# Kernel tuning notes

Hardware: AMD Instinct MI355X
Metric: run time of the kernel (lower is better)

The kernel has to match this reference:

```python
import jax, jax.numpy as jnp
import numpy as np

B, S, D_SEQ, D_ITEM, A, H = 2048, 200, 256, 64, 128, 1
HD = A // H
SCALE = A ** 0.5


def prelu(x, a):
    return jnp.where(x >= 0, x, a * x)


def setup_inputs() -> dict:
    key = jax.random.key(0)
    ks = jax.random.split(key, 10)
    inp = {
        "transformer_out": jax.random.normal(ks[0], (B, S, D_SEQ), dtype=jnp.float32),
        "mask": jax.random.randint(ks[1], (B, S), 0, 2, dtype=jnp.int32),  # 1 = pad
        "target_item_emb": jax.random.normal(ks[2], (B, D_ITEM), dtype=jnp.float32),
        # parameters (torch Linear weight layout: [out, in])
        "W_q": jax.random.normal(ks[3], (A, D_ITEM), dtype=jnp.float32) * (1.0 / np.sqrt(D_ITEM)),
        "W_k": jax.random.normal(ks[4], (A, D_SEQ), dtype=jnp.float32) * (1.0 / np.sqrt(D_SEQ)),
        "W_v": jax.random.normal(ks[5], (A, D_SEQ), dtype=jnp.float32) * (1.0 / np.sqrt(D_SEQ)),
        "W_kernel": jnp.eye(HD, dtype=jnp.float32),
        "ffn_W": jax.random.normal(ks[6], (D_SEQ, A), dtype=jnp.float32) * (1.0 / np.sqrt(A)),
        "ffn_b": jnp.zeros((D_SEQ,), dtype=jnp.float32),
        "prelu_a": jnp.asarray(0.25, dtype=jnp.float32),  # shared PReLU(1) param
    }
    return inp


def reference(transformer_out, mask, target_item_emb, W_q, W_k, W_v, W_kernel, ffn_W, ffn_b, prelu_a):
    # Q/K/V projections + shared PReLU activation
    K = prelu(jnp.einsum('bsd,ad->bsa', transformer_out, W_k), prelu_a)   # [B,S,A]
    V = prelu(jnp.einsum('bsd,ad->bsa', transformer_out, W_v), prelu_a)   # [B,S,A]
    Q = prelu(jnp.einsum('bd,ad->ba', target_item_emb, W_q), prelu_a)     # [B,A]

    # split heads
    Kh = K.reshape(B, S, H, HD)          # [B,S,H,hd]
    Vh = V.reshape(B, S, H, HD)
    Qh = Q.reshape(B, H, HD)             # [B,H,hd]

    # bilinear attention score: K W Q^T / sqrt(attn_dim)
    score = jnp.einsum('bshd,dc,bhc->bhs', Kh, W_kernel, Qh) / SCALE      # [B,H,S]

    # mask: input mask 1=pad; valid = 1-mask; padded positions -> -1e9
    valid = (1 - mask).astype(jnp.float32)[:, None, :]                     # [B,1,S]
    score = jnp.where(valid == 0, -1e9, score)

    attn = jax.nn.softmax(score, axis=-1)                                  # [B,H,S]

    # weighted sum of values, merge heads
    out = jnp.einsum('bhs,bshd->bhd', attn, Vh).reshape(B, H * HD)         # [B,A]

    ffn_out = prelu(out @ ffn_W.T + ffn_b, prelu_a)                        # [B,D_SEQ]
    return ffn_out, attn
```

## Files before the change

kernel.cpp:

```cpp
#include <hip/hip_runtime.h>
#include <hip/hip_bf16.h>

#define NB    2048
#define SS    200
#define DSEQ  256
#define DITEM 64
#define AA    128
#define NS    4

typedef __bf16 bf16x8 __attribute__((ext_vector_type(8)));
typedef float  f32x4  __attribute__((ext_vector_type(4)));

__device__ __forceinline__ float prelu_f(float x, float a) { return x >= 0.f ? x : a * x; }

#define ROR_F(x, n) __int_as_float(__builtin_amdgcn_update_dpp(0, __float_as_int(x), 0x120 + (n), 0xf, 0xf, true))
__device__ __forceinline__ float row_sum16(float x) {
    x += ROR_F(x, 1); x += ROR_F(x, 2); x += ROR_F(x, 4); x += ROR_F(x, 8);
    return x;
}
__device__ __forceinline__ float row_max16(float x) {
    x = fmaxf(x, ROR_F(x, 1)); x = fmaxf(x, ROR_F(x, 2));
    x = fmaxf(x, ROR_F(x, 4)); x = fmaxf(x, ROR_F(x, 8));
    return x;
}

__global__ void prep_kernel(const float* __restrict__ Wk, const float* __restrict__ Wv,
                            __hip_bfloat16* __restrict__ Wb) {
    int idx = blockIdx.x * 256 + threadIdx.x;
    int a = idx >> 8, d = idx & 255;
    float v = (a < 128) ? Wk[a * 256 + d] : Wv[(a - 128) * 256 + d];
    int boff = (d * 2) ^ ((a & 7) << 4);
    Wb[a * 256 + (boff >> 1)] = __float2bfloat16(v);
}

#define ISSUE_R(tt, s, L, H)                                                    \
    {                                                                           \
        int r_ = idx_lds[s][(tt) * 16 + srow];                                  \
        const float* xp_ = X + ((size_t)(b0 + (s)) * SS + r_) * DSEQ + chunk * 8; \
        L = *reinterpret_cast<const f32x4*>(xp_);                               \
        H = *reinterpret_cast<const f32x4*>(xp_ + 4);                           \
    }

#define STAGE_R(tt, s, L, H)                                                    \
    {                                                                           \
        bf16x8 v_;                                                              \
        v_[0] = (__bf16)L[0]; v_[1] = (__bf16)L[1];                             \
        v_[2] = (__bf16)L[2]; v_[3] = (__bf16)L[3];                             \
        v_[4] = (__bf16)H[0]; v_[5] = (__bf16)H[1];                             \
        v_[6] = (__bf16)H[2]; v_[7] = (__bf16)H[3];                             \
        *reinterpret_cast<bf16x8*>(xbase + (s) * 16384 + ((tt) & 1) * 8192 + wr_off) = v_; \
    }

#define SMFOLD(tp, s)                                                           \
    {                                                                           \
        const int q_ = (tp) & 1;                                                \
        const int s0_ = (tp) * 16;                                              \
        f32x4 r0_ = *reinterpret_cast<const f32x4*>(&sp[s][q_][c][0]);          \
        f32x4 r1_ = *reinterpret_cast<const f32x4*>(&sp[s][q_][c][4]);          \
        float sc_ = (r0_[0]+r0_[1]+r0_[2]+r0_[3]+r1_[0]+r1_[1]+r1_[2]+r1_[3]) * inv_scale; \
        sc_ = (s0_ + c < nv##s) ? sc_ : -1e9f;                                  \
        if (tid < 16 && s0_ + tid < nv##s) arena[s][idx_lds[s][s0_ + tid]] = sc_; \
        float tmax_ = row_max16(sc_);                                           \
        float nm_ = fmaxf(m##s, tmax_);                                         \
        float fs_ = __expf(m##s - nm_);                                         \
        float e_  = __expf(sc_ - nm_);                                          \
        float ls_ = row_sum16(e_);                                              \
        l##s = l##s * fs_ + ls_; m##s = nm_;                                    \
        oacc##s *= fs_;                                                         \
        _Pragma("unroll")                                                       \
        for (int i_ = 0; i_ < 4; i_++) {                                        \
            float ew_ = __shfl(e_, (lane & 48) | (rg * 4 + i_), 64);            \
            oacc##s += ew_ * prelu_f(aVp##s[i_], pa);                           \
        }                                                                       \
    }

#define CHALF(k0)                                                               \
    _Pragma("unroll")                                                           \
    for (int k = (k0); k < (k0) + 4; k++) {                                     \
        const int o = (k * 64 + rg * 16) ^ rswz;                                \
        bf16x8 bk  = *reinterpret_cast<const bf16x8*>(kb + o);                  \
        bf16x8 bv  = *reinterpret_cast<const bf16x8*>(vb + o);                  \
        bf16x8 af0 = *reinterpret_cast<const bf16x8*>(rb0 + o);                 \
        bf16x8 af1 = *reinterpret_cast<const bf16x8*>(rb1 + o);                 \
        bf16x8 af2 = *reinterpret_cast<const bf16x8*>(rb2 + o);                 \
        bf16x8 af3 = *reinterpret_cast<const bf16x8*>(rb3 + o);                 \
        aK0 = __builtin_amdgcn_mfma_f32_16x16x32_bf16(af0, bk, aK0, 0, 0, 0);   \
        aVp0 = __builtin_amdgcn_mfma_f32_16x16x32_bf16(af0, bv, aVp0, 0, 0, 0); \
        aK1 = __builtin_amdgcn_mfma_f32_16x16x32_bf16(af1, bk, aK1, 0, 0, 0);   \
        aVp1 = __builtin_amdgcn_mfma_f32_16x16x32_bf16(af1, bv, aVp1, 0, 0, 0); \
        aK2 = __builtin_amdgcn_mfma_f32_16x16x32_bf16(af2, bk, aK2, 0, 0, 0);   \
        aVp2 = __builtin_amdgcn_mfma_f32_16x16x32_bf16(af2, bv, aVp2, 0, 0, 0); \
        aK3 = __builtin_amdgcn_mfma_f32_16x16x32_bf16(af3, bk, aK3, 0, 0, 0);   \
        aVp3 = __builtin_amdgcn_mfma_f32_16x16x32_bf16(af3, bv, aVp3, 0, 0, 0); \
    }

#define SCOREPART(tt, s)                                                        \
    {                                                                           \
        float pr_[4];                                                           \
        _Pragma("unroll")                                                       \
        for (int i = 0; i < 4; i++) pr_[i] = row_sum16(prelu_f(aK##s[i], pa) * uw##s); \
        if (c == 0) {                                                           \
            _Pragma("unroll")                                                   \
            for (int i = 0; i < 4; i++) sp[s][(tt) & 1][rg * 4 + i][w] = pr_[i]; \
        }                                                                       \
    }

__global__ __launch_bounds__(512, 2)
void pool_main(
    const float* __restrict__ X,
    const int*   __restrict__ maskp,
    const float* __restrict__ temb,
    const float* __restrict__ Wq,
    const float* __restrict__ Wker,
    const float* __restrict__ ffnW,
    const float* __restrict__ ffnb,
    const float* __restrict__ prelu_a,
    const __hip_bfloat16* __restrict__ Wb,
    float* __restrict__ out)
{
    __shared__ __hip_bfloat16 Xt[NS][2][16][256];
    __shared__ float sp[NS][2][16][8];
    __shared__ float arena[NS][336];
    __shared__ int   idx_lds[NS][208];
    __shared__ int   nvt[NS];

    const int tid  = threadIdx.x;
    const int w    = tid >> 6;
    const int lane = tid & 63;
    const int c    = lane & 15;
    const int rg   = lane >> 4;
    const int b0   = blockIdx.x * NS;
    const float pa = *prelu_a;
    const float inv_scale = 0.08838834764831845f;

    const int srow  = tid >> 5;
    const int chunk = tid & 31;
    const int wr_off = srow * 512 + ((chunk * 16) ^ ((srow & 7) << 4));
    char* xbase = (char*)&Xt[0][0][0][0];
    const int rswz = (c & 7) << 4;

    const char* kb = (const char*)Wb + (size_t)(16 * w + c) * 512;
    const char* vb = kb + 65536;

    if (w < NS) {
        int base = 0;
        #pragma unroll
        for (int ch = 0; ch < 4; ch++) {
            int pos = ch * 64 + lane;
            bool val = (pos < SS) && (maskp[(size_t)(b0 + w) * SS + pos] == 0);
            unsigned long long ball = __ballot(val);
            int pre = __popcll(ball & ((1ull << lane) - 1));
            if (val) idx_lds[w][base + pre] = pos;
            base += (int)__popcll(ball);
        }
        asm volatile("s_waitcnt lgkmcnt(0)" ::: "memory");
        int safe = (base > 0) ? idx_lds[w][base - 1] : 0;
        for (int j = base + lane; j < 208; j += 64) idx_lds[w][j] = safe;
        if (lane == 0) nvt[w] = base;
    }
    const int ps = tid >> 7;
    const int po = tid & 127;
    if (po < DITEM) arena[ps][po] = temb[(size_t)(b0 + ps) * DITEM + po];
    __syncthreads();

    f32x4 p0lo, p0hi, p1lo, p1hi, p2lo, p2hi, p3lo, p3hi;
    ISSUE_R(0, 0, p0lo, p0hi); ISSUE_R(0, 1, p1lo, p1hi);
    ISSUE_R(0, 2, p2lo, p2hi); ISSUE_R(0, 3, p3lo, p3hi);

    {
        float acc = 0.f;
        #pragma unroll
        for (int d4 = 0; d4 < 16; d4++) {
            f32x4 tv = *reinterpret_cast<const f32x4*>(&arena[ps][d4 * 4]);
            f32x4 wq4 = *reinterpret_cast<const f32x4*>(Wq + (size_t)po * DITEM + d4 * 4);
            acc += wq4[0]*tv[0] + wq4[1]*tv[1] + wq4[2]*tv[2] + wq4[3]*tv[3];
        }
        arena[ps][64 + po] = prelu_f(acc, pa);
    }
    __syncthreads();

    {
        float acc = 0.f;
        #pragma unroll
        for (int d4 = 0; d4 < 32; d4++) {
            f32x4 qv = *reinterpret_cast<const f32x4*>(&arena[ps][64 + d4 * 4]);
            f32x4 wk4 = *reinterpret_cast<const f32x4*>(Wker + (size_t)po * AA + d4 * 4);
            acc += wk4[0]*qv[0] + wk4[1]*qv[1] + wk4[2]*qv[2] + wk4[3]*qv[3];
        }
        arena[ps][192 + po] = acc;
    }
    __syncthreads();
    const float uw0 = arena[0][192 + 16 * w + c];
    const float uw1 = arena[1][192 + 16 * w + c];
    const float uw2 = arena[2][192 + 16 * w + c];
    const float uw3 = arena[3][192 + 16 * w + c];
    const int nv0 = nvt[0], nv1 = nvt[1], nv2 = nvt[2], nv3 = nvt[3];
    int ntmax = (nv0 + 15) >> 4;
    { int n1 = (nv1 + 15) >> 4; if (n1 > ntmax) ntmax = n1; }
    { int n2 = (nv2 + 15) >> 4; if (n2 > ntmax) ntmax = n2; }
    { int n3 = (nv3 + 15) >> 4; if (n3 > ntmax) ntmax = n3; }
    if (ntmax < 1) ntmax = 1;

    if (tid < 208) {
        arena[0][tid] = -1e9f; arena[1][tid] = -1e9f;
        arena[2][tid] = -1e9f; arena[3][tid] = -1e9f;
    }

    STAGE_R(0, 0, p0lo, p0hi); STAGE_R(0, 1, p1lo, p1hi);
    STAGE_R(0, 2, p2lo, p2hi); STAGE_R(0, 3, p3lo, p3hi);
    __syncthreads();

    float m0 = -INFINITY, l0 = 0.f, oacc0 = 0.f;
    float m1 = -INFINITY, l1 = 0.f, oacc1 = 0.f;
    float m2 = -INFINITY, l2 = 0.f, oacc2 = 0.f;
    float m3 = -INFINITY, l3 = 0.f, oacc3 = 0.f;
    f32x4 aVp0 = {0.f,0.f,0.f,0.f}, aVp1 = {0.f,0.f,0.f,0.f};
    f32x4 aVp2 = {0.f,0.f,0.f,0.f}, aVp3 = {0.f,0.f,0.f,0.f};
    f32x4 stAlo, stAhi, stBlo, stBhi;

    for (int t = 0; t < ntmax; t++) {
        const int more = (t + 1 < ntmax);

        if (more) { ISSUE_R(t + 1, 0, stAlo, stAhi); ISSUE_R(t + 1, 1, stBlo, stBhi); }

        if (t > 0) { SMFOLD(t - 1, 0); SMFOLD(t - 1, 1); SMFOLD(t - 1, 2); SMFOLD(t - 1, 3); }
        aVp0 = (f32x4){0.f,0.f,0.f,0.f}; aVp1 = (f32x4){0.f,0.f,0.f,0.f};
        aVp2 = (f32x4){0.f,0.f,0.f,0.f}; aVp3 = (f32x4){0.f,0.f,0.f,0.f};

        const char* rb0 = xbase + 0 * 16384 + (t & 1) * 8192 + c * 512;
        const char* rb1 = xbase + 1 * 16384 + (t & 1) * 8192 + c * 512;
        const char* rb2 = xbase + 2 * 16384 + (t & 1) * 8192 + c * 512;
        const char* rb3 = xbase + 3 * 16384 + (t & 1) * 8192 + c * 512;
        f32x4 aK0 = {0.f,0.f,0.f,0.f}, aK1 = {0.f,0.f,0.f,0.f};
        f32x4 aK2 = {0.f,0.f,0.f,0.f}, aK3 = {0.f,0.f,0.f,0.f};

        CHALF(0);

        if (more) {
            STAGE_R(t + 1, 0, stAlo, stAhi); ISSUE_R(t + 1, 2, stAlo, stAhi);
            STAGE_R(t + 1, 1, stBlo, stBhi); ISSUE_R(t + 1, 3, stBlo, stBhi);
        }

        CHALF(4);

        SCOREPART(t, 0); SCOREPART(t, 1); SCOREPART(t, 2); SCOREPART(t, 3);

        if (more) { STAGE_R(t + 1, 2, stAlo, stAhi); STAGE_R(t + 1, 3, stBlo, stBhi); }
        __syncthreads();
    }

    {
        const int tl = ntmax - 1;
        SMFOLD(tl, 0); SMFOLD(tl, 1); SMFOLD(tl, 2); SMFOLD(tl, 3);
    }

    oacc0 += __shfl_xor(oacc0, 16, 64); oacc0 += __shfl_xor(oacc0, 32, 64);
    oacc1 += __shfl_xor(oacc1, 16, 64); oacc1 += __shfl_xor(oacc1, 32, 64);
    oacc2 += __shfl_xor(oacc2, 16, 64); oacc2 += __shfl_xor(oacc2, 32, 64);
    oacc3 += __shfl_xor(oacc3, 16, 64); oacc3 += __shfl_xor(oacc3, 32, 64);
    const float invl0 = 1.0f / l0, invl1 = 1.0f / l1;
    const float invl2 = 1.0f / l2, invl3 = 1.0f / l3;
    if (lane < 16) {
        arena[0][208 + 16 * w + lane] = oacc0 * invl0;
        arena[1][208 + 16 * w + lane] = oacc1 * invl1;
        arena[2][208 + 16 * w + lane] = oacc2 * invl2;
        arena[3][208 + 16 * w + lane] = oacc3 * invl3;
    }
    __syncthreads();

    if (tid < SS) {
        out[(size_t)NB * DSEQ + (size_t)(b0 + 0) * SS + tid] = __expf(arena[0][tid] - m0) * invl0;
        out[(size_t)NB * DSEQ + (size_t)(b0 + 1) * SS + tid] = __expf(arena[1][tid] - m1) * invl1;
        out[(size_t)NB * DSEQ + (size_t)(b0 + 2) * SS + tid] = __expf(arena[2][tid] - m2) * invl2;
        out[(size_t)NB * DSEQ + (size_t)(b0 + 3) * SS + tid] = __expf(arena[3][tid] - m3) * invl3;
    }

    {
        const int o  = tid & 255;
        const int sA = tid >> 8;
        float accA = ffnb[o], accB = accA;
        #pragma unroll 8
        for (int a4 = 0; a4 < 32; a4++) {
            f32x4 wv4 = *reinterpret_cast<const f32x4*>(ffnW + (size_t)o * AA + a4 * 4);
            f32x4 ovA = *reinterpret_cast<const f32x4*>(&arena[sA][208 + a4 * 4]);
            f32x4 ovB = *reinterpret_cast<const f32x4*>(&arena[sA + 2][208 + a4 * 4]);
            accA += wv4[0]*ovA[0] + wv4[1]*ovA[1] + wv4[2]*ovA[2] + wv4[3]*ovA[3];
            accB += wv4[0]*ovB[0] + wv4[1]*ovB[1] + wv4[2]*ovB[2] + wv4[3]*ovB[3];
        }
        out[(size_t)(b0 + sA) * DSEQ + o]     = prelu_f(accA, pa);
        out[(size_t)(b0 + sA + 2) * DSEQ + o] = prelu_f(accB, pa);
    }
}

extern "C" void kernel_launch(void* const* d_in, const int* in_sizes, int n_in,
                              void* d_out, int out_size, void* d_ws, size_t ws_size,
                              hipStream_t stream) {
    const float* X    = (const float*)d_in[0];
    const int*   mask = (const int*)  d_in[1];
    const float* temb = (const float*)d_in[2];
    const float* Wq   = (const float*)d_in[3];
    const float* Wk   = (const float*)d_in[4];
    const float* Wv   = (const float*)d_in[5];
    const float* Wker = (const float*)d_in[6];
    const float* ffnW = (const float*)d_in[7];
    const float* ffnb = (const float*)d_in[8];
    const float* pa   = (const float*)d_in[9];
    float* out = (float*)d_out;

    __hip_bfloat16* Wb = (__hip_bfloat16*)d_ws;

    prep_kernel<<<256, 256, 0, stream>>>(Wk, Wv, Wb);
    pool_main<<<NB / NS, 512, 0, stream>>>(X, mask, temb, Wq, Wker, ffnW, ffnb, pa, Wb, out);
}
```

Before: 116.6 us.

## Split fused pooling kernel into projection pass and separate softmax/FFN kernel

Removes the online softmax and value accumulation from the projection kernel. The first kernel now writes raw scores and PReLU'd V tiles as bf16 to a workspace. A second per-batch kernel does the masked softmax, the weighted V sum and the FFN. This shortens the main kernel's critical loop and register pressure, at the cost of an extra launch and about 100MB of V written to and reread from global memory.

```diff
diff --git a/kernel.cpp b/kernel.cpp
--- a/kernel.cpp
+++ b/kernel.cpp
@@ -7,8 +7,10 @@
 #define DITEM 64
 #define AA    128
 #define NS    4
+#define MAXNT 13
 
 typedef __bf16 bf16x8 __attribute__((ext_vector_type(8)));
+typedef __bf16 bf16x4 __attribute__((ext_vector_type(4)));
 typedef float  f32x4  __attribute__((ext_vector_type(4)));
 
 __device__ __forceinline__ float prelu_f(float x, float a) { return x >= 0.f ? x : a * x; }
@@ -16,11 +18,6 @@
 #define ROR_F(x, n) __int_as_float(__builtin_amdgcn_update_dpp(0, __float_as_int(x), 0x120 + (n), 0xf, 0xf, true))
 __device__ __forceinline__ float row_sum16(float x) {
     x += ROR_F(x, 1); x += ROR_F(x, 2); x += ROR_F(x, 4); x += ROR_F(x, 8);
-    return x;
-}
-__device__ __forceinline__ float row_max16(float x) {
-    x = fmaxf(x, ROR_F(x, 1)); x = fmaxf(x, ROR_F(x, 2));
-    x = fmaxf(x, ROR_F(x, 4)); x = fmaxf(x, ROR_F(x, 8));
     return x;
 }
 
@@ -49,29 +46,6 @@
         v_[4] = (__bf16)H[0]; v_[5] = (__bf16)H[1];                             \
         v_[6] = (__bf16)H[2]; v_[7] = (__bf16)H[3];                             \
         *reinterpret_cast<bf16x8*>(xbase + (s) * 16384 + ((tt) & 1) * 8192 + wr_off) = v_; \
-    }
-
-#define SMFOLD(tp, s)                                                           \
-    {                                                                           \
-        const int q_ = (tp) & 1;                                                \
-        const int s0_ = (tp) * 16;                                              \
-        f32x4 r0_ = *reinterpret_cast<const f32x4*>(&sp[s][q_][c][0]);          \
-        f32x4 r1_ = *reinterpret_cast<const f32x4*>(&sp[s][q_][c][4]);          \
-        float sc_ = (r0_[0]+r0_[1]+r0_[2]+r0_[3]+r1_[0]+r1_[1]+r1_[2]+r1_[3]) * inv_scale; \
-        sc_ = (s0_ + c < nv##s) ? sc_ : -1e9f;                                  \
-        if (tid < 16 && s0_ + tid < nv##s) arena[s][idx_lds[s][s0_ + tid]] = sc_; \
-        float tmax_ = row_max16(sc_);                                           \
-        float nm_ = fmaxf(m##s, tmax_);                                         \
-        float fs_ = __expf(m##s - nm_);                                         \
-        float e_  = __expf(sc_ - nm_);                                          \
-        float ls_ = row_sum16(e_);                                              \
-        l##s = l##s * fs_ + ls_; m##s = nm_;                                    \
-        oacc##s *= fs_;                                                         \
-        _Pragma("unroll")                                                       \
-        for (int i_ = 0; i_ < 4; i_++) {                                        \
-            float ew_ = __shfl(e_, (lane & 48) | (rg * 4 + i_), 64);            \
-            oacc##s += ew_ * prelu_f(aVp##s[i_], pa);                           \
-        }                                                                       \
     }
 
 #define CHALF(k0)                                                               \
@@ -85,13 +59,13 @@
         bf16x8 af2 = *reinterpret_cast<const bf16x8*>(rb2 + o);                 \
         bf16x8 af3 = *reinterpret_cast<const bf16x8*>(rb3 + o);                 \
         aK0 = __builtin_amdgcn_mfma_f32_16x16x32_bf16(af0, bk, aK0, 0, 0, 0);   \
-        aVp0 = __builtin_amdgcn_mfma_f32_16x16x32_bf16(af0, bv, aVp0, 0, 0, 0); \
+        aV0 = __builtin_amdgcn_mfma_f32_16x16x32_bf16(af0, bv, aV0, 0, 0, 0);   \
         aK1 = __builtin_amdgcn_mfma_f32_16x16x32_bf16(af1, bk, aK1, 0, 0, 0);   \
-        aVp1 = __builtin_amdgcn_mfma_f32_16x16x32_bf16(af1, bv, aVp1, 0, 0, 0); \
+        aV1 = __builtin_amdgcn_mfma_f32_16x16x32_bf16(af1, bv, aV1, 0, 0, 0);   \
         aK2 = __builtin_amdgcn_mfma_f32_16x16x32_bf16(af2, bk, aK2, 0, 0, 0);   \
-        aVp2 = __builtin_amdgcn_mfma_f32_16x16x32_bf16(af2, bv, aVp2, 0, 0, 0); \
+        aV2 = __builtin_amdgcn_mfma_f32_16x16x32_bf16(af2, bv, aV2, 0, 0, 0);   \
         aK3 = __builtin_amdgcn_mfma_f32_16x16x32_bf16(af3, bk, aK3, 0, 0, 0);   \
-        aVp3 = __builtin_amdgcn_mfma_f32_16x16x32_bf16(af3, bv, aVp3, 0, 0, 0); \
+        aV3 = __builtin_amdgcn_mfma_f32_16x16x32_bf16(af3, bv, aV3, 0, 0, 0);   \
     }
 
 #define SCOREPART(tt, s)                                                        \
@@ -105,18 +79,37 @@
         }                                                                       \
     }
 
+#define VSTORE(tt, s)                                                           \
+    {                                                                           \
+        bf16x4 vv_;                                                             \
+        vv_[0] = (__bf16)prelu_f(aV##s[0], pa);                                 \
+        vv_[1] = (__bf16)prelu_f(aV##s[1], pa);                                 \
+        vv_[2] = (__bf16)prelu_f(aV##s[2], pa);                                 \
+        vv_[3] = (__bf16)prelu_f(aV##s[3], pa);                                 \
+        *reinterpret_cast<bf16x4*>(Vbuf + ((size_t)(b0 + (s)) * MAXNT + (tt)) * 4096 \
+                                   + w * 512 + lane * 8) = vv_;                 \
+    }
+
+#define SCSUM(tp)                                                               \
+    if (w < NS && lane < 16) {                                                  \
+        const int q_ = (tp) & 1;                                                \
+        f32x4 r0_ = *reinterpret_cast<const f32x4*>(&sp[w][q_][lane][0]);       \
+        f32x4 r1_ = *reinterpret_cast<const f32x4*>(&sp[w][q_][lane][4]);       \
+        scores_ws[(size_t)(b0 + w) * 208 + (tp) * 16 + lane] =                  \
+            r0_[0]+r0_[1]+r0_[2]+r0_[3]+r1_[0]+r1_[1]+r1_[2]+r1_[3];            \
+    }
+
 __global__ __launch_bounds__(512, 2)
-void pool_main(
+void proj_a(
     const float* __restrict__ X,
     const int*   __restrict__ maskp,
     const float* __restrict__ temb,
     const float* __restrict__ Wq,
     const float* __restrict__ Wker,
-    const float* __restrict__ ffnW,
-    const float* __restrict__ ffnb,
     const float* __restrict__ prelu_a,
     const __hip_bfloat16* __restrict__ Wb,
-    float* __restrict__ out)
+    float* __restrict__ scores_ws,
+    char*  __restrict__ Vbuf)
 {
     __shared__ __hip_bfloat16 Xt[NS][2][16][256];
     __shared__ float sp[NS][2][16][8];
@@ -131,7 +124,6 @@
     const int rg   = lane >> 4;
     const int b0   = blockIdx.x * NS;
     const float pa = *prelu_a;
-    const float inv_scale = 0.08838834764831845f;
 
     const int srow  = tid >> 5;
     const int chunk = tid & 31;
@@ -201,21 +193,10 @@
     { int n3 = (nv3 + 15) >> 4; if (n3 > ntmax) ntmax = n3; }
     if (ntmax < 1) ntmax = 1;
 
-    if (tid < 208) {
-        arena[0][tid] = -1e9f; arena[1][tid] = -1e9f;
-        arena[2][tid] = -1e9f; arena[3][tid] = -1e9f;
-    }
-
     STAGE_R(0, 0, p0lo, p0hi); STAGE_R(0, 1, p1lo, p1hi);
     STAGE_R(0, 2, p2lo, p2hi); STAGE_R(0, 3, p3lo, p3hi);
     __syncthreads();
 
-    float m0 = -INFINITY, l0 = 0.f, oacc0 = 0.f;
-    float m1 = -INFINITY, l1 = 0.f, oacc1 = 0.f;
-    float m2 = -INFINITY, l2 = 0.f, oacc2 = 0.f;
-    float m3 = -INFINITY, l3 = 0.f, oacc3 = 0.f;
-    f32x4 aVp0 = {0.f,0.f,0.f,0.f}, aVp1 = {0.f,0.f,0.f,0.f};
-    f32x4 aVp2 = {0.f,0.f,0.f,0.f}, aVp3 = {0.f,0.f,0.f,0.f};
     f32x4 stAlo, stAhi, stBlo, stBhi;
 
     for (int t = 0; t < ntmax; t++) {
@@ -223,9 +204,7 @@
 
         if (more) { ISSUE_R(t + 1, 0, stAlo, stAhi); ISSUE_R(t + 1, 1, stBlo, stBhi); }
 
-        if (t > 0) { SMFOLD(t - 1, 0); SMFOLD(t - 1, 1); SMFOLD(t - 1, 2); SMFOLD(t - 1, 3); }
-        aVp0 = (f32x4){0.f,0.f,0.f,0.f}; aVp1 = (f32x4){0.f,0.f,0.f,0.f};
-        aVp2 = (f32x4){0.f,0.f,0.f,0.f}; aVp3 = (f32x4){0.f,0.f,0.f,0.f};
+        if (t > 0) SCSUM(t - 1);
 
         const char* rb0 = xbase + 0 * 16384 + (t & 1) * 8192 + c * 512;
         const char* rb1 = xbase + 1 * 16384 + (t & 1) * 8192 + c * 512;
@@ -233,6 +212,8 @@
         const char* rb3 = xbase + 3 * 16384 + (t & 1) * 8192 + c * 512;
         f32x4 aK0 = {0.f,0.f,0.f,0.f}, aK1 = {0.f,0.f,0.f,0.f};
         f32x4 aK2 = {0.f,0.f,0.f,0.f}, aK3 = {0.f,0.f,0.f,0.f};
+        f32x4 aV0 = {0.f,0.f,0.f,0.f}, aV1 = {0.f,0.f,0.f,0.f};
+        f32x4 aV2 = {0.f,0.f,0.f,0.f}, aV3 = {0.f,0.f,0.f,0.f};
 
         CHALF(0);
 
@@ -244,52 +225,105 @@
         CHALF(4);
 
         SCOREPART(t, 0); SCOREPART(t, 1); SCOREPART(t, 2); SCOREPART(t, 3);
+        VSTORE(t, 0); VSTORE(t, 1); VSTORE(t, 2); VSTORE(t, 3);
 
         if (more) { STAGE_R(t + 1, 2, stAlo, stAhi); STAGE_R(t + 1, 3, stBlo, stBhi); }
         __syncthreads();
     }
 
-    {
-        const int tl = ntmax - 1;
-        SMFOLD(tl, 0); SMFOLD(tl, 1); SMFOLD(tl, 2); SMFOLD(tl, 3);
-    }
-
-    oacc0 += __shfl_xor(oacc0, 16, 64); oacc0 += __shfl_xor(oacc0, 32, 64);
-    oacc1 += __shfl_xor(oacc1, 16, 64); oacc1 += __shfl_xor(oacc1, 32, 64);
-    oacc2 += __shfl_xor(oacc2, 16, 64); oacc2 += __shfl_xor(oacc2, 32, 64);
-    oacc3 += __shfl_xor(oacc3, 16, 64); oacc3 += __shfl_xor(oacc3, 32, 64);
-    const float invl0 = 1.0f / l0, invl1 = 1.0f / l1;
-    const float invl2 = 1.0f / l2, invl3 = 1.0f / l3;
-    if (lane < 16) {
-        arena[0][208 + 16 * w + lane] = oacc0 * invl0;
-        arena[1][208 + 16 * w + lane] = oacc1 * invl1;
-        arena[2][208 + 16 * w + lane] = oacc2 * invl2;
-        arena[3][208 + 16 * w + lane] = oacc3 * invl3;
-    }
-    __syncthreads();
+    SCSUM(ntmax - 1);
+}
+
+__global__ __launch_bounds__(256)
+void attn_ffn_b(
+    const int*   __restrict__ maskp,
+    const float* __restrict__ scores_ws,
+    const char*  __restrict__ Vbuf,
+    const float* __restrict__ ffnW,
+    const float* __restrict__ ffnb,
+    const float* __restrict__ prelu_a,
+    float* __restrict__ out)
+{
+    __shared__ int   idx[208];
+    __shared__ int   inv[208];
+    __shared__ int   nv_s;
+    __shared__ float ebuf[208];
+    __shared__ float ovec[AA];
+    __shared__ float red[256];
+    __shared__ float wr1[4], wr2[4];
+
+    const int b = blockIdx.x, tid = threadIdx.x;
+    const int w = tid >> 6, lane = tid & 63;
+    const float pa = *prelu_a;
+    const float inv_scale = 0.08838834764831845f;
+
+    if (w == 0) {
+        int base = 0;
+        #pragma unroll
+        for (int ch = 0; ch < 4; ch++) {
+            int pos = ch * 64 + lane;
+            bool val = (pos < SS) && (maskp[(size_t)b * SS + pos] == 0);
+            unsigned long long ball = __ballot(val);
+            int pre = __popcll(ball & ((1ull << lane) - 1));
+            if (val) { idx[base + pre] = pos; inv[pos] = base + pre; }
+            base += (int)__popcll(ball);
+        }
+        if (lane == 0) nv_s = base;
+    }
+    __syncthreads();
+    const int nv = nv_s;
+
+    float sc = -3e38f;
+    if (tid < nv) sc = scores_ws[(size_t)b * 208 + tid] * inv_scale;
+    float v = sc;
+    #pragma unroll
+    for (int o = 1; o < 64; o <<= 1) v = fmaxf(v, __shfl_xor(v, o, 64));
+    if (lane == 0) wr1[w] = v;
+    __syncthreads();
+    const float m = fmaxf(fmaxf(wr1[0], wr1[1]), fmaxf(wr1[2], wr1[3]));
+    float e = (tid < nv) ? __expf(sc - m) : 0.f;
+    if (tid < 208) ebuf[tid] = e;
+    float sv = e;
+    #pragma unroll
+    for (int o = 1; o < 64; o <<= 1) sv += __shfl_xor(sv, o, 64);
+    if (lane == 0) wr2[w] = sv;
+    __syncthreads();
+    const float l = wr2[0] + wr2[1] + wr2[2] + wr2[3];
+    const float invl = 1.0f / l;
 
     if (tid < SS) {
-        out[(size_t)NB * DSEQ + (size_t)(b0 + 0) * SS + tid] = __expf(arena[0][tid] - m0) * invl0;
-        out[(size_t)NB * DSEQ + (size_t)(b0 + 1) * SS + tid] = __expf(arena[1][tid] - m1) * invl1;
-        out[(size_t)NB * DSEQ + (size_t)(b0 + 2) * SS + tid] = __expf(arena[2][tid] - m2) * invl2;
-        out[(size_t)NB * DSEQ + (size_t)(b0 + 3) * SS + tid] = __expf(arena[3][tid] - m3) * invl3;
-    }
-
-    {
-        const int o  = tid & 255;
-        const int sA = tid >> 8;
-        float accA = ffnb[o], accB = accA;
-        #pragma unroll 8
-        for (int a4 = 0; a4 < 32; a4++) {
-            f32x4 wv4 = *reinterpret_cast<const f32x4*>(ffnW + (size_t)o * AA + a4 * 4);
-            f32x4 ovA = *reinterpret_cast<const f32x4*>(&arena[sA][208 + a4 * 4]);
-            f32x4 ovB = *reinterpret_cast<const f32x4*>(&arena[sA + 2][208 + a4 * 4]);
-            accA += wv4[0]*ovA[0] + wv4[1]*ovA[1] + wv4[2]*ovA[2] + wv4[3]*ovA[3];
-            accB += wv4[0]*ovB[0] + wv4[1]*ovB[1] + wv4[2]*ovB[2] + wv4[3]*ovB[3];
-        }
-        out[(size_t)(b0 + sA) * DSEQ + o]     = prelu_f(accA, pa);
-        out[(size_t)(b0 + sA + 2) * DSEQ + o] = prelu_f(accB, pa);
-    }
+        int mk = maskp[(size_t)b * SS + tid];
+        out[(size_t)NB * DSEQ + (size_t)b * SS + tid] = mk ? 0.f : ebuf[inv[tid]] * invl;
+    }
+
+    const int nt = (nv + 15) >> 4;
+    const int a = tid & 127, h = tid >> 7;
+    const int t0 = h ? (nt >> 1) : 0;
+    const int t1 = h ? nt : (nt >> 1);
+    const char* vbase = Vbuf + (size_t)b * MAXNT * 4096 + (a >> 4) * 512 + (a & 15) * 8;
+    float acc = 0.f;
+    for (int t = t0; t < t1; t++) {
+        #pragma unroll
+        for (int rg = 0; rg < 4; rg++) {
+            bf16x4 vv = *reinterpret_cast<const bf16x4*>(vbase + (size_t)t * 4096 + rg * 128);
+            const int s = t * 16 + rg * 4;
+            acc += ebuf[s]     * (float)vv[0] + ebuf[s + 1] * (float)vv[1]
+                 + ebuf[s + 2] * (float)vv[2] + ebuf[s + 3] * (float)vv[3];
+        }
+    }
+    red[tid] = acc;
+    __syncthreads();
+    if (tid < AA) ovec[tid] = (red[tid] + red[tid + 128]) * invl;
+    __syncthreads();
+
+    float facc = ffnb[tid];
+    #pragma unroll 8
+    for (int a4 = 0; a4 < 32; a4++) {
+        f32x4 ov = *reinterpret_cast<const f32x4*>(&ovec[a4 * 4]);
+        f32x4 wv = *reinterpret_cast<const f32x4*>(ffnW + (size_t)tid * AA + a4 * 4);
+        facc += wv[0]*ov[0] + wv[1]*ov[1] + wv[2]*ov[2] + wv[3]*ov[3];
+    }
+    out[(size_t)b * DSEQ + tid] = prelu_f(facc, pa);
 }
 
 extern "C" void kernel_launch(void* const* d_in, const int* in_sizes, int n_in,
@@ -307,8 +341,12 @@
     const float* pa   = (const float*)d_in[9];
     float* out = (float*)d_out;
 
-    __hip_bfloat16* Wb = (__hip_bfloat16*)d_ws;
+    char* ws = (char*)d_ws;
+    __hip_bfloat16* Wb = (__hip_bfloat16*)ws;
+    char*  Vbuf      = ws + 131072;
+    float* scores_ws = (float*)(ws + 131072 + (size_t)NB * MAXNT * 4096);
 
     prep_kernel<<<256, 256, 0, stream>>>(Wk, Wv, Wb);
-    pool_main<<<NB / NS, 512, 0, stream>>>(X, mask, temb, Wq, Wker, ffnW, ffnb, pa, Wb, out);
-}
+    proj_a<<<NB / NS, 512, 0, stream>>>(X, mask, temb, Wq, Wker, pa, Wb, scores_ws, Vbuf);
+    attn_ffn_b<<<NB, 256, 0, stream>>>(mask, scores_ws, Vbuf, ffnW, ffnb, pa, out);
+}
```

Measured after the change: 134.4 us. +15.2%, slower.
